# Kernel tuning notes

Hardware: AMD Instinct MI355X
Metric: run time of the kernel (lower is better)

The kernel has to match this reference:

```python
import jax, jax.numpy as jnp
import numpy as np

DIM, N_HEAD, DK, DV = 1024, 16, 64, 64
B, S = 1, 4096


def setup_inputs() -> dict:
    key = jax.random.key(0)
    ks = jax.random.split(key, 9)
    sd = 0.02
    return {
        "x": jax.random.normal(ks[0], (B, S, DIM), dtype=jnp.float32),
        "Wq": jax.random.normal(ks[1], (DIM, N_HEAD * DK), dtype=jnp.float32) * sd,
        "bq": jnp.zeros((N_HEAD * DK,), dtype=jnp.float32),
        "Wk": jax.random.normal(ks[2], (DIM, N_HEAD * DK), dtype=jnp.float32) * sd,
        "bk": jnp.zeros((N_HEAD * DK,), dtype=jnp.float32),
        "Wv": jax.random.normal(ks[3], (DIM, N_HEAD * DV), dtype=jnp.float32) * sd,
        "bv": jnp.zeros((N_HEAD * DV,), dtype=jnp.float32),
        "Wo": jax.random.normal(ks[4], (N_HEAD * DV, DIM), dtype=jnp.float32) * sd,
        "bo": jnp.zeros((DIM,), dtype=jnp.float32),
    }


def reference(x, Wq, bq, Wk, bk, Wv, bv, Wo, bo):
    b, s, _ = x.shape
    scale = DK ** (-0.5)
    # projections -> [b, h, s, d]
    q = (x @ Wq + bq).reshape(b, s, N_HEAD, DK).transpose(0, 2, 1, 3)
    k = (x @ Wk + bk).reshape(b, s, N_HEAD, DK).transpose(0, 2, 1, 3)
    v = (x @ Wv + bv).reshape(b, s, N_HEAD, DV).transpose(0, 2, 1, 3)
    attn = jnp.einsum("bhqd,bhkd->bhqk", q, k) * scale  # [b,h,s,s]
    attn = jax.nn.softmax(attn, axis=-1)
    out = jnp.einsum("bhqk,bhkd->bhqd", attn, v)  # [b,h,s,dv]
    out = out.transpose(0, 2, 1, 3).reshape(b, s, N_HEAD * DV)
    return out @ Wo + bo
```

## Files before the change

### kernel.cpp

```cpp
#include <hip/hip_runtime.h>
#include <hip/hip_bf16.h>
#include <hip/hip_fp16.h>

#define SEQ 4096
#define DIM 1024
#define NH 16
#define NT (SEQ / 64)

typedef __attribute__((ext_vector_type(4))) float f32x4;
typedef __attribute__((ext_vector_type(16))) float f32x16;
typedef __attribute__((ext_vector_type(8))) _Float16 half8;
typedef __attribute__((ext_vector_type(4))) _Float16 half4;

#if __has_builtin(__builtin_amdgcn_exp2f)
#define EXP2(x) __builtin_amdgcn_exp2f(x)
#else
#define EXP2(x) exp2f(x)
#endif

#define SMC 0.18033688f

__global__ __launch_bounds__(256) void prep_all(const float* __restrict__ x,
                                                _Float16* __restrict__ xh,
                                                const float* __restrict__ W0,
                                                const float* __restrict__ W1,
                                                const float* __restrict__ W2,
                                                const float* __restrict__ W3,
                                                _Float16* __restrict__ T0,
                                                _Float16* __restrict__ T1,
                                                _Float16* __restrict__ T2,
                                                _Float16* __restrict__ T3) {
  if (blockIdx.z == 4) {
    const int blkid = blockIdx.x * 32 + blockIdx.y;
#pragma unroll
    for (int u = 0; u < 4; u++) {
      int i = blkid * 4096 + u * 1024 + threadIdx.x * 4;
      float4 v = *reinterpret_cast<const float4*>(x + i);
      half4 h;
      h[0] = (_Float16)v.x; h[1] = (_Float16)v.y;
      h[2] = (_Float16)v.z; h[3] = (_Float16)v.w;
      *reinterpret_cast<half4*>(xh + i) = h;
    }
    return;
  }
  const float* W = blockIdx.z == 0 ? W0 : blockIdx.z == 1 ? W1 : blockIdx.z == 2 ? W2 : W3;
  _Float16* Wt = blockIdx.z == 0 ? T0 : blockIdx.z == 1 ? T1 : blockIdx.z == 2 ? T2 : T3;
  __shared__ float t[32][33];
  int bx = blockIdx.x * 32;
  int by = blockIdx.y * 32;
  int tx = threadIdx.x & 31, ty = threadIdx.x >> 5;
#pragma unroll
  for (int i = 0; i < 4; i++)
    t[ty + i * 8][tx] = W[(by + ty + i * 8) * DIM + bx + tx];
  __syncthreads();
#pragma unroll
  for (int i = 0; i < 4; i++)
    Wt[(bx + ty + i * 8) * DIM + by + tx] = (_Float16)t[tx][ty + i * 8];
}

template <int MODE>
__device__ __forceinline__ void gemm_body(const _Float16* __restrict__ A,
                                          const _Float16* __restrict__ Bt,
                                          const float* __restrict__ bias,
                                          void* __restrict__ outp,
                                          int M, int N, int Kd, int bmb, int bnb) {
  __shared__ __align__(16) _Float16 As[64][72];
  __shared__ __align__(16) _Float16 Bs[128][72];
  const int tid = threadIdx.x, lane = tid & 63, w = tid >> 6;
  const int bm = bmb * 64, bn = bnb * 128;
  const int l15 = lane & 15, g = lane >> 4, kb = g * 8;
  const int sra = tid >> 2, sca = (tid & 3) * 16;
  const int srb = tid >> 1, scb = (tid & 1) * 32;
  f32x4 acc[4][2] = {};

  uint4 ar0, ar1, br0, br1, br2, br3;
  auto LOADT = [&](int k0) {
    const _Float16* ap = A + (size_t)(bm + sra) * Kd + k0 + sca;
    ar0 = *reinterpret_cast<const uint4*>(ap);
    ar1 = *reinterpret_cast<const uint4*>(ap + 8);
    const _Float16* bp = Bt + (size_t)(bn + srb) * Kd + k0 + scb;
    br0 = *reinterpret_cast<const uint4*>(bp);
    br1 = *reinterpret_cast<const uint4*>(bp + 8);
    br2 = *reinterpret_cast<const uint4*>(bp + 16);
    br3 = *reinterpret_cast<const uint4*>(bp + 24);
  };

  LOADT(0);
  for (int k0 = 0; k0 < Kd; k0 += 64) {
    __syncthreads();
    *reinterpret_cast<uint4*>(&As[sra][sca]) = ar0;
    *reinterpret_cast<uint4*>(&As[sra][sca + 8]) = ar1;
    *reinterpret_cast<uint4*>(&Bs[srb][scb]) = br0;
    *reinterpret_cast<uint4*>(&Bs[srb][scb + 8]) = br1;
    *reinterpret_cast<uint4*>(&Bs[srb][scb + 16]) = br2;
    *reinterpret_cast<uint4*>(&Bs[srb][scb + 24]) = br3;
    __syncthreads();
    if (k0 + 64 < Kd) LOADT(k0 + 64);
#pragma unroll
    for (int kk = 0; kk < 64; kk += 32) {
      half8 af[4], bf[2];
#pragma unroll
      for (int i = 0; i < 4; i++)
        af[i] = *reinterpret_cast<const half8*>(&As[i * 16 + l15][kk + kb]);
#pragma unroll
      for (int j = 0; j < 2; j++)
        bf[j] = *reinterpret_cast<const half8*>(&Bs[w * 32 + j * 16 + l15][kk + kb]);
      __builtin_amdgcn_s_setprio(1);
#pragma unroll
      for (int i = 0; i < 4; i++)
#pragma unroll
        for (int j = 0; j < 2; j++)
          acc[i][j] = __builtin_amdgcn_mfma_f32_16x16x32_f16(af[i], bf[j], acc[i][j], 0, 0, 0);
      __builtin_amdgcn_s_setprio(0);
    }
  }

  const int gswap = ((g & 1) << 1) | (g >> 1);
#pragma unroll
  for (int i = 0; i < 4; i++)
#pragma unroll
    for (int j = 0; j < 2; j++) {
      const int col = bn + w * 32 + j * 16 + l15;
      if (MODE == 2) {
        const int rowP = bm + i * 16 + gswap * 4;
        half4 hv;
#pragma unroll
        for (int r = 0; r < 4; r++) hv[r] = (_Float16)(acc[i][j][r] + bias[col]);
        *reinterpret_cast<half4*>(&((_Float16*)outp)[(size_t)col * M + rowP]) = hv;
      } else {
        const int row0 = bm + i * 16 + g * 4;
#pragma unroll
        for (int r = 0; r < 4; r++) {
          float vv = acc[i][j][r] + bias[col];
          if (MODE == 0) {
            _Float16* O = (_Float16*)outp;
            O[(((col >> 6) * SEQ) + row0 + r) * 64 + (col & 63)] = (_Float16)vv;
          } else {
            float* O = (float*)outp;
            O[(size_t)(row0 + r) * N + col] = vv;
          }
        }
      }
    }
}

__global__ __launch_bounds__(256) void gemm_qkv(const _Float16* __restrict__ A,
                                                const _Float16* __restrict__ WqT,
                                                const _Float16* __restrict__ WkT,
                                                const _Float16* __restrict__ WvT,
                                                const float* __restrict__ bq,
                                                const float* __restrict__ bk,
                                                const float* __restrict__ bv,
                                                _Float16* __restrict__ Qd,
                                                _Float16* __restrict__ Kd,
                                                _Float16* __restrict__ Vd) {
  if (blockIdx.z == 0)
    gemm_body<0>(A, WqT, bq, (void*)Qd, SEQ, DIM, DIM, blockIdx.x, blockIdx.y);
  else if (blockIdx.z == 1)
    gemm_body<0>(A, WkT, bk, (void*)Kd, SEQ, DIM, DIM, blockIdx.x, blockIdx.y);
  else
    gemm_body<2>(A, WvT, bv, (void*)Vd, SEQ, DIM, DIM, blockIdx.x, blockIdx.y);
}

__global__ __launch_bounds__(256) void gemm_out(const _Float16* __restrict__ A,
                                                const _Float16* __restrict__ Bt,
                                                const float* __restrict__ bias,
                                                float* __restrict__ out) {
  gemm_body<1>(A, Bt, bias, (void*)out, SEQ, DIM, DIM, blockIdx.x, blockIdx.y);
}

__global__ __launch_bounds__(256) void attn_fwd(const _Float16* __restrict__ Q,
                                                const _Float16* __restrict__ Kh,
                                                const _Float16* __restrict__ Vt_g,
                                                _Float16* __restrict__ Og) {
  __shared__ __align__(16) _Float16 Ks[3][64][72];
  __shared__ __align__(16) _Float16 Vs[3][64][72];
  const int hh = blockIdx.y;
  const int q0 = blockIdx.x * 128;
  const int tid = threadIdx.x, lane = tid & 63, w = tid >> 6;
  const int l31 = lane & 31, hq = lane >> 5, h8 = hq * 8;

  const int qrow = q0 + w * 32 + l31;
  const _Float16* qp = Q + ((size_t)hh * SEQ + qrow) * 64;
  half8 qf[4];
#pragma unroll
  for (int d = 0; d < 4; d++)
    qf[d] = *reinterpret_cast<const half8*>(qp + d * 16 + h8);

  f32x16 o[2] = {};
  float m = -1e30f, lsum = 0.f, negmC = 1e30f;
  const f32x16 kZero16 = {};

  const int srow = tid >> 3, sc8 = (tid & 7) * 8;
  const _Float16* kbase = Kh + (size_t)hh * SEQ * 64;
  const _Float16* vbase = Vt_g + (size_t)hh * 64 * SEQ;

  uint4 kr0, kr1, vr0, vr1;
  auto LOADKV = [&](int kt2) {
    const _Float16* kp = kbase + (size_t)(kt2 * 64 + srow) * 64 + sc8;
    kr0 = *reinterpret_cast<const uint4*>(kp);
    kr1 = *reinterpret_cast<const uint4*>(kp + 32 * 64);
    const _Float16* vp = vbase + (size_t)srow * SEQ + kt2 * 64 + sc8;
    vr0 = *reinterpret_cast<const uint4*>(vp);
    vr1 = *reinterpret_cast<const uint4*>(vp + 32 * SEQ);
  };
  auto STAGE = [&](int buf) {
    *reinterpret_cast<uint4*>(&Ks[buf][srow][sc8]) = kr0;
    *reinterpret_cast<uint4*>(&Ks[buf][srow + 32][sc8]) = kr1;
    *reinterpret_cast<uint4*>(&Vs[buf][srow][sc8]) = vr0;
    *reinterpret_cast<uint4*>(&Vs[buf][srow + 32][sc8]) = vr1;
  };

  auto QK = [&](int tile, f32x16 (&sf)[2]) {
    const int b = tile % 3;
    __builtin_amdgcn_s_setprio(1);
    {
      half8 kf0 = *reinterpret_cast<const half8*>(&Ks[b][l31][h8]);
      half8 kf1 = *reinterpret_cast<const half8*>(&Ks[b][32 + l31][h8]);
      sf[0] = __builtin_amdgcn_mfma_f32_32x32x16_f16(kf0, qf[0], kZero16, 0, 0, 0);
      sf[1] = __builtin_amdgcn_mfma_f32_32x32x16_f16(kf1, qf[0], kZero16, 0, 0, 0);
    }
#pragma unroll
    for (int d = 1; d < 4; d++) {
      half8 kf0 = *reinterpret_cast<const half8*>(&Ks[b][l31][d * 16 + h8]);
      half8 kf1 = *reinterpret_cast<const half8*>(&Ks[b][32 + l31][d * 16 + h8]);
      sf[0] = __builtin_amdgcn_mfma_f32_32x32x16_f16(kf0, qf[d], sf[0], 0, 0, 0);
      sf[1] = __builtin_amdgcn_mfma_f32_32x32x16_f16(kf1, qf[d], sf[1], 0, 0, 0);
    }
    __builtin_amdgcn_s_setprio(0);
  };

  auto ITER = [&](int t, f32x16 (&scur)[2], f32x16 (&snext)[2]) {
    if (t + 1 < NT) QK(t + 1, snext);

    float pm = scur[0][0];
#pragma unroll
    for (int r = 1; r < 16; r++) pm = fmaxf(pm, scur[0][r]);
#pragma unroll
    for (int r = 0; r < 16; r++) pm = fmaxf(pm, scur[1][r]);
    if (__any(pm > m + 64.f)) {
      pm = fmaxf(pm, __shfl_xor(pm, 32, 64));
      float mn = fmaxf(m, pm);
      float al = EXP2((m - mn) * SMC);
      m = mn;
      negmC = -mn * SMC;
      lsum *= al;
      o[0] *= al;
      o[1] *= al;
    }
    f32x16 pf0, pf1;
#pragma unroll
    for (int r = 0; r < 16; r++) {
      float p = EXP2(fmaf(scur[0][r], SMC, negmC));
      pf0[r] = p;
      lsum += p;
    }
#pragma unroll
    for (int r = 0; r < 16; r++) {
      float p = EXP2(fmaf(scur[1][r], SMC, negmC));
      pf1[r] = p;
      lsum += p;
    }
    half8 pb[4];
#pragma unroll
    for (int s = 0; s < 4; s++) {
      const int base = (s & 1) * 8;
      unsigned d0, d1, d2, d3;
      if (s < 2) {
        d0 = __builtin_bit_cast(unsigned, __builtin_amdgcn_cvt_pkrtz(pf0[base + 0], pf0[base + 1]));
        d1 = __builtin_bit_cast(unsigned, __builtin_amdgcn_cvt_pkrtz(pf0[base + 2], pf0[base + 3]));
        d2 = __builtin_bit_cast(unsigned, __builtin_amdgcn_cvt_pkrtz(pf0[base + 4], pf0[base + 5]));
        d3 = __builtin_bit_cast(unsigned, __builtin_amdgcn_cvt_pkrtz(pf0[base + 6], pf0[base + 7]));
      } else {
        d0 = __builtin_bit_cast(unsigned, __builtin_amdgcn_cvt_pkrtz(pf1[base + 0], pf1[base + 1]));
        d1 = __builtin_bit_cast(unsigned, __builtin_amdgcn_cvt_pkrtz(pf1[base + 2], pf1[base + 3]));
        d2 = __builtin_bit_cast(unsigned, __builtin_amdgcn_cvt_pkrtz(pf1[base + 4], pf1[base + 5]));
        d3 = __builtin_bit_cast(unsigned, __builtin_amdgcn_cvt_pkrtz(pf1[base + 6], pf1[base + 7]));
      }
      uint4 uu = {d0, d1, d2, d3};
      pb[s] = __builtin_bit_cast(half8, uu);
    }

    const int bv = t % 3;
    __builtin_amdgcn_s_setprio(1);
#pragma unroll
    for (int s = 0; s < 4; s++) {
      half8 va0 = *reinterpret_cast<const half8*>(&Vs[bv][l31][s * 16 + h8]);
      half8 va1 = *reinterpret_cast<const half8*>(&Vs[bv][32 + l31][s * 16 + h8]);
      o[0] = __builtin_amdgcn_mfma_f32_32x32x16_f16(va0, pb[s], o[0], 0, 0, 0);
      o[1] = __builtin_amdgcn_mfma_f32_32x32x16_f16(va1, pb[s], o[1], 0, 0, 0);
    }
    __builtin_amdgcn_s_setprio(0);

    if (t + 2 < NT) STAGE((t + 2) % 3);
    if (t + 3 < NT) LOADKV(t + 3);
    __syncthreads();
  };

  LOADKV(0); STAGE(0);
  LOADKV(1); STAGE(1);
  LOADKV(2);
  __syncthreads();

  f32x16 sfA[2], sfB[2];
  QK(0, sfA);
  for (int t = 0; t < NT; t += 2) {
    ITER(t, sfA, sfB);
    ITER(t + 1, sfB, sfA);
  }

  float ls = lsum + __shfl_xor(lsum, 32, 64);
  float rinv = 1.f / ls;
#pragma unroll
  for (int tile = 0; tile < 2; tile++)
#pragma unroll
    for (int rg = 0; rg < 4; rg++) {
      half4 hv;
#pragma unroll
      for (int j = 0; j < 4; j++) hv[j] = (_Float16)(o[tile][rg * 4 + j] * rinv);
      const int dv = tile * 32 + rg * 8 + 4 * hq;
      *reinterpret_cast<half4*>(&Og[(size_t)qrow * DIM + hh * 64 + dv]) = hv;
    }
}


extern "C" void kernel_launch(void* const* d_in, const int* in_sizes, int n_in,
                              void* d_out, int out_size, void* d_ws, size_t ws_size,
                              hipStream_t stream) {
  const float* x  = (const float*)d_in[0];
  const float* Wq = (const float*)d_in[1];
  const float* bq = (const float*)d_in[2];
  const float* Wk = (const float*)d_in[3];
  const float* bk = (const float*)d_in[4];
  const float* Wv = (const float*)d_in[5];
  const float* bv = (const float*)d_in[6];
  const float* Wo = (const float*)d_in[7];
  const float* bo = (const float*)d_in[8];

  char* ws = (char*)d_ws;
  _Float16* xh  = (_Float16*)ws;
  _Float16* WqT = (_Float16*)(ws + (size_t)SEQ * DIM * 2);
  _Float16* WkT = WqT + DIM * DIM;
  _Float16* WvT = WkT + DIM * DIM;
  _Float16* WoT = WvT + DIM * DIM;
  _Float16* Qd  = WoT + DIM * DIM;
  _Float16* Kd  = Qd + (size_t)SEQ * DIM;
  _Float16* Vd  = Kd + (size_t)SEQ * DIM;
  _Float16* Od  = Vd + (size_t)SEQ * DIM;

  prep_all<<<dim3(32, 32, 5), 256, 0, stream>>>(x, xh, Wq, Wk, Wv, Wo,
                                                WqT, WkT, WvT, WoT);

  gemm_qkv<<<dim3(SEQ / 64, DIM / 128, 3), 256, 0, stream>>>(
      xh, WqT, WkT, WvT, bq, bk, bv, Qd, Kd, Vd);

  attn_fwd<<<dim3(SEQ / 128, NH), 256, 0, stream>>>(Qd, Kd, Vd, Od);

  gemm_out<<<dim3(SEQ / 64, DIM / 128), 256, 0, stream>>>(Od, WoT, bo, (float*)d_out);
}
```

Baseline: 171.1 us.

## Split attention over key range and merge partial results in separate kernel

Attention is split into two halves along the key/value sequence through a third grid dimension. Each half writes unnormalized fp32 partial outputs plus its running max and sum to workspace, and a new merge kernel rescales, combines and normalizes them into the fp16 head output. The goal is more blocks and shorter per-block loops to improve CU utilization. In exchange it adds an extra launch and roughly 32 MB of fp32 partial traffic. The K/V LDS row padding also changes from 72 to 70 halves, which breaks 16-byte alignment of the vector LDS reads.

```diff
diff --git a/kernel.cpp b/kernel.cpp
--- a/kernel.cpp
+++ b/kernel.cpp
@@ -6,6 +6,8 @@
 #define DIM 1024
 #define NH 16
 #define NT (SEQ / 64)
+#define NSPLIT 2
+#define TPP (NT / NSPLIT)
 
 typedef __attribute__((ext_vector_type(4))) float f32x4;
 typedef __attribute__((ext_vector_type(16))) float f32x16;
@@ -172,10 +174,12 @@
 __global__ __launch_bounds__(256) void attn_fwd(const _Float16* __restrict__ Q,
                                                 const _Float16* __restrict__ Kh,
                                                 const _Float16* __restrict__ Vt_g,
-                                                _Float16* __restrict__ Og) {
-  __shared__ __align__(16) _Float16 Ks[3][64][72];
-  __shared__ __align__(16) _Float16 Vs[3][64][72];
+                                                float* __restrict__ Op,
+                                                float2* __restrict__ Ml) {
+  __shared__ __align__(16) _Float16 Ks[3][64][70];
+  __shared__ __align__(16) _Float16 Vs[3][64][70];
   const int hh = blockIdx.y;
+  const int part = blockIdx.z;
   const int q0 = blockIdx.x * 128;
   const int tid = threadIdx.x, lane = tid & 63, w = tid >> 6;
   const int l31 = lane & 31, hq = lane >> 5, h8 = hq * 8;
@@ -230,8 +234,10 @@
     __builtin_amdgcn_s_setprio(0);
   };
 
+  const int t0 = part * TPP, t1 = t0 + TPP;
+
   auto ITER = [&](int t, f32x16 (&scur)[2], f32x16 (&snext)[2]) {
-    if (t + 1 < NT) QK(t + 1, snext);
+    if (t + 1 < t1) QK(t + 1, snext);
 
     float pm = scur[0][0];
 #pragma unroll
@@ -292,35 +298,62 @@
     }
     __builtin_amdgcn_s_setprio(0);
 
-    if (t + 2 < NT) STAGE((t + 2) % 3);
-    if (t + 3 < NT) LOADKV(t + 3);
+    if (t + 2 < t1) STAGE((t + 2) % 3);
+    if (t + 3 < t1) LOADKV(t + 3);
     __syncthreads();
   };
 
-  LOADKV(0); STAGE(0);
-  LOADKV(1); STAGE(1);
-  LOADKV(2);
+  LOADKV(t0); STAGE(t0 % 3);
+  LOADKV(t0 + 1); STAGE((t0 + 1) % 3);
+  LOADKV(t0 + 2);
   __syncthreads();
 
   f32x16 sfA[2], sfB[2];
-  QK(0, sfA);
-  for (int t = 0; t < NT; t += 2) {
+  QK(t0, sfA);
+  for (int t = t0; t < t1; t += 2) {
     ITER(t, sfA, sfB);
     ITER(t + 1, sfB, sfA);
   }
 
   float ls = lsum + __shfl_xor(lsum, 32, 64);
-  float rinv = 1.f / ls;
+  const size_t prow = ((size_t)part * NH + hh) * SEQ + qrow;
 #pragma unroll
   for (int tile = 0; tile < 2; tile++)
 #pragma unroll
     for (int rg = 0; rg < 4; rg++) {
-      half4 hv;
-#pragma unroll
-      for (int j = 0; j < 4; j++) hv[j] = (_Float16)(o[tile][rg * 4 + j] * rinv);
+      float4 ov;
+      ov.x = o[tile][rg * 4 + 0];
+      ov.y = o[tile][rg * 4 + 1];
+      ov.z = o[tile][rg * 4 + 2];
+      ov.w = o[tile][rg * 4 + 3];
       const int dv = tile * 32 + rg * 8 + 4 * hq;
-      *reinterpret_cast<half4*>(&Og[(size_t)qrow * DIM + hh * 64 + dv]) = hv;
-    }
+      *reinterpret_cast<float4*>(&Op[prow * 64 + dv]) = ov;
+    }
+  if (hq == 0) Ml[prow] = make_float2(m, ls);
+}
+
+__global__ __launch_bounds__(256) void attn_merge(const float* __restrict__ Op,
+                                                  const float2* __restrict__ Ml,
+                                                  _Float16* __restrict__ Og) {
+  const int gid = blockIdx.x * 256 + threadIdx.x;
+  const int dv4 = (gid & 15) * 4;
+  const int row = gid >> 4;
+  const int h = row >> 12, s = row & (SEQ - 1);
+  float2 a = Ml[row];
+  float2 b = Ml[(size_t)NH * SEQ + row];
+  float mm = fmaxf(a.x, b.x);
+  float e1 = EXP2((a.x - mm) * SMC);
+  float e2 = EXP2((b.x - mm) * SMC);
+  float rinv = 1.f / (a.y * e1 + b.y * e2);
+  e1 *= rinv; e2 *= rinv;
+  float4 o1 = *reinterpret_cast<const float4*>(&Op[(size_t)row * 64 + dv4]);
+  float4 o2 = *reinterpret_cast<const float4*>(&Op[((size_t)NH * SEQ + row) * 64 + dv4]);
+  half4 hv;
+  hv[0] = (_Float16)(o1.x * e1 + o2.x * e2);
+  hv[1] = (_Float16)(o1.y * e1 + o2.y * e2);
+  hv[2] = (_Float16)(o1.z * e1 + o2.z * e2);
+  hv[3] = (_Float16)(o1.w * e1 + o2.w * e2);
+  *reinterpret_cast<half4*>(&Og[(size_t)s * DIM + h * 64 + dv4]) = hv;
 }
 
 
@@ -347,6 +380,8 @@
   _Float16* Kd  = Qd + (size_t)SEQ * DIM;
   _Float16* Vd  = Kd + (size_t)SEQ * DIM;
   _Float16* Od  = Vd + (size_t)SEQ * DIM;
+  float*    Opart = (float*)(Od + (size_t)SEQ * DIM);
+  float2*   Mlp   = (float2*)(Opart + (size_t)NSPLIT * NH * SEQ * 64);
 
   prep_all<<<dim3(32, 32, 5), 256, 0, stream>>>(x, xh, Wq, Wk, Wv, Wo,
                                                 WqT, WkT, WvT, WoT);
@@ -354,7 +389,8 @@
   gemm_qkv<<<dim3(SEQ / 64, DIM / 128, 3), 256, 0, stream>>>(
       xh, WqT, WkT, WvT, bq, bk, bv, Qd, Kd, Vd);
 
-  attn_fwd<<<dim3(SEQ / 128, NH), 256, 0, stream>>>(Qd, Kd, Vd, Od);
+  attn_fwd<<<dim3(SEQ / 128, NH, NSPLIT), 256, 0, stream>>>(Qd, Kd, Vd, Opart, Mlp);
+  attn_merge<<<(NH * SEQ * 16) / 256, 256, 0, stream>>>(Opart, Mlp, Od);
 
   gemm_out<<<dim3(SEQ / 64, DIM / 128), 256, 0, stream>>>(Od, WoT, bo, (float*)d_out);
 }
```

Measured after the change: 188.8 us. +10.3%, slower.

## Compute softmax row sums with ones-vector MFMA and interleave exp with PV

Applied to the files above, without the earlier changes.

Replaces the scalar per-lane accumulation of softmax row sums with an extra MFMA that multiplies a ones vector by the half-precision probabilities, so the sum comes out of the matrix unit. It also restructures the row max into a tree reduction and interleaves the exp/convert of each 16-column slice with its PV MFMAs instead of computing all probabilities first. The aim is to cut VALU work and register pressure and to overlap exp with MFMA. The cost is one extra MFMA per slice, 16 more accumulator registers, and row sums now taken from fp16-rounded probabilities.

```diff
diff --git a/kernel.cpp b/kernel.cpp
--- a/kernel.cpp
+++ b/kernel.cpp
@@ -188,8 +188,11 @@
     qf[d] = *reinterpret_cast<const half8*>(qp + d * 16 + h8);
 
   f32x16 o[2] = {};
-  float m = -1e30f, lsum = 0.f, negmC = 1e30f;
+  f32x16 ol = {};
+  float m = -1e30f, negmC = 1e30f;
   const f32x16 kZero16 = {};
+  const _Float16 one1 = (_Float16)1.f;
+  const half8 kOnes8 = {one1, one1, one1, one1, one1, one1, one1, one1};
 
   const int srow = tid >> 3, sc8 = (tid & 7) * 8;
   const _Float16* kbase = Kh + (size_t)hh * SEQ * 64;
@@ -233,64 +236,72 @@
   auto ITER = [&](int t, f32x16 (&scur)[2], f32x16 (&snext)[2]) {
     if (t + 1 < NT) QK(t + 1, snext);
 
-    float pm = scur[0][0];
-#pragma unroll
-    for (int r = 1; r < 16; r++) pm = fmaxf(pm, scur[0][r]);
-#pragma unroll
-    for (int r = 0; r < 16; r++) pm = fmaxf(pm, scur[1][r]);
+    float t0 = fmaxf(fmaxf(scur[0][0], scur[0][1]), scur[0][2]);
+    float t1 = fmaxf(fmaxf(scur[0][3], scur[0][4]), scur[0][5]);
+    float t2 = fmaxf(fmaxf(scur[0][6], scur[0][7]), scur[0][8]);
+    float t3 = fmaxf(fmaxf(scur[0][9], scur[0][10]), scur[0][11]);
+    float t4 = fmaxf(fmaxf(scur[0][12], scur[0][13]), scur[0][14]);
+    float t5 = fmaxf(fmaxf(scur[0][15], scur[1][0]), scur[1][1]);
+    float t6 = fmaxf(fmaxf(scur[1][2], scur[1][3]), scur[1][4]);
+    float t7 = fmaxf(fmaxf(scur[1][5], scur[1][6]), scur[1][7]);
+    float t8 = fmaxf(fmaxf(scur[1][8], scur[1][9]), scur[1][10]);
+    float t9 = fmaxf(fmaxf(scur[1][11], scur[1][12]), scur[1][13]);
+    float ta = fmaxf(scur[1][14], scur[1][15]);
+    float u0 = fmaxf(fmaxf(t0, t1), t2);
+    float u1 = fmaxf(fmaxf(t3, t4), t5);
+    float u2 = fmaxf(fmaxf(t6, t7), t8);
+    float u3 = fmaxf(t9, ta);
+    float pm = fmaxf(fmaxf(fmaxf(u0, u1), u2), u3);
     if (__any(pm > m + 64.f)) {
       pm = fmaxf(pm, __shfl_xor(pm, 32, 64));
       float mn = fmaxf(m, pm);
       float al = EXP2((m - mn) * SMC);
       m = mn;
       negmC = -mn * SMC;
-      lsum *= al;
+      ol *= al;
       o[0] *= al;
       o[1] *= al;
     }
-    f32x16 pf0, pf1;
-#pragma unroll
-    for (int r = 0; r < 16; r++) {
-      float p = EXP2(fmaf(scur[0][r], SMC, negmC));
-      pf0[r] = p;
-      lsum += p;
-    }
-#pragma unroll
-    for (int r = 0; r < 16; r++) {
-      float p = EXP2(fmaf(scur[1][r], SMC, negmC));
-      pf1[r] = p;
-      lsum += p;
-    }
-    half8 pb[4];
+
+    const int bv = t % 3;
 #pragma unroll
     for (int s = 0; s < 4; s++) {
       const int base = (s & 1) * 8;
-      unsigned d0, d1, d2, d3;
+      float p0, p1, p2, p3, p4, p5, p6, p7;
       if (s < 2) {
-        d0 = __builtin_bit_cast(unsigned, __builtin_amdgcn_cvt_pkrtz(pf0[base + 0], pf0[base + 1]));
-        d1 = __builtin_bit_cast(unsigned, __builtin_amdgcn_cvt_pkrtz(pf0[base + 2], pf0[base + 3]));
-        d2 = __builtin_bit_cast(unsigned, __builtin_amdgcn_cvt_pkrtz(pf0[base + 4], pf0[base + 5]));
-        d3 = __builtin_bit_cast(unsigned, __builtin_amdgcn_cvt_pkrtz(pf0[base + 6], pf0[base + 7]));
+        p0 = EXP2(fmaf(scur[0][base + 0], SMC, negmC));
+        p1 = EXP2(fmaf(scur[0][base + 1], SMC, negmC));
+        p2 = EXP2(fmaf(scur[0][base + 2], SMC, negmC));
+        p3 = EXP2(fmaf(scur[0][base + 3], SMC, negmC));
+        p4 = EXP2(fmaf(scur[0][base + 4], SMC, negmC));
+        p5 = EXP2(fmaf(scur[0][base + 5], SMC, negmC));
+        p6 = EXP2(fmaf(scur[0][base + 6], SMC, negmC));
+        p7 = EXP2(fmaf(scur[0][base + 7], SMC, negmC));
       } else {
-        d0 = __builtin_bit_cast(unsigned, __builtin_amdgcn_cvt_pkrtz(pf1[base + 0], pf1[base + 1]));
-        d1 = __builtin_bit_cast(unsigned, __builtin_amdgcn_cvt_pkrtz(pf1[base + 2], pf1[base + 3]));
-        d2 = __builtin_bit_cast(unsigned, __builtin_amdgcn_cvt_pkrtz(pf1[base + 4], pf1[base + 5]));
-        d3 = __builtin_bit_cast(unsigned, __builtin_amdgcn_cvt_pkrtz(pf1[base + 6], pf1[base + 7]));
+        p0 = EXP2(fmaf(scur[1][base + 0], SMC, negmC));
+        p1 = EXP2(fmaf(scur[1][base + 1], SMC, negmC));
+        p2 = EXP2(fmaf(scur[1][base + 2], SMC, negmC));
+        p3 = EXP2(fmaf(scur[1][base + 3], SMC, negmC));
+        p4 = EXP2(fmaf(scur[1][base + 4], SMC, negmC));
+        p5 = EXP2(fmaf(scur[1][base + 5], SMC, negmC));
+        p6 = EXP2(fmaf(scur[1][base + 6], SMC, negmC));
+        p7 = EXP2(fmaf(scur[1][base + 7], SMC, negmC));
       }
+      unsigned d0 = __builtin_bit_cast(unsigned, __builtin_amdgcn_cvt_pkrtz(p0, p1));
+      unsigned d1 = __builtin_bit_cast(unsigned, __builtin_amdgcn_cvt_pkrtz(p2, p3));
+      unsigned d2 = __builtin_bit_cast(unsigned, __builtin_amdgcn_cvt_pkrtz(p4, p5));
+      unsigned d3 = __builtin_bit_cast(unsigned, __builtin_amdgcn_cvt_pkrtz(p6, p7));
       uint4 uu = {d0, d1, d2, d3};
-      pb[s] = __builtin_bit_cast(half8, uu);
-    }
-
-    const int bv = t % 3;
-    __builtin_amdgcn_s_setprio(1);
-#pragma unroll
-    for (int s = 0; s < 4; s++) {
+      half8 pbs = __builtin_bit_cast(half8, uu);
+
       half8 va0 = *reinterpret_cast<const half8*>(&Vs[bv][l31][s * 16 + h8]);
       half8 va1 = *reinterpret_cast<const half8*>(&Vs[bv][32 + l31][s * 16 + h8]);
-      o[0] = __builtin_amdgcn_mfma_f32_32x32x16_f16(va0, pb[s], o[0], 0, 0, 0);
-      o[1] = __builtin_amdgcn_mfma_f32_32x32x16_f16(va1, pb[s], o[1], 0, 0, 0);
-    }
-    __builtin_amdgcn_s_setprio(0);
+      __builtin_amdgcn_s_setprio(1);
+      o[0] = __builtin_amdgcn_mfma_f32_32x32x16_f16(va0, pbs, o[0], 0, 0, 0);
+      o[1] = __builtin_amdgcn_mfma_f32_32x32x16_f16(va1, pbs, o[1], 0, 0, 0);
+      ol = __builtin_amdgcn_mfma_f32_32x32x16_f16(kOnes8, pbs, ol, 0, 0, 0);
+      __builtin_amdgcn_s_setprio(0);
+    }
 
     if (t + 2 < NT) STAGE((t + 2) % 3);
     if (t + 3 < NT) LOADKV(t + 3);
@@ -309,8 +320,7 @@
     ITER(t + 1, sfB, sfA);
   }
 
-  float ls = lsum + __shfl_xor(lsum, 32, 64);
-  float rinv = 1.f / ls;
+  float rinv = 1.f / ol[0];
 #pragma unroll
   for (int tile = 0; tile < 2; tile++)
 #pragma unroll
```

New measurement: 204.4 us. +19.4%, slower.
